# Optimization experiments

Hardware: AMD Instinct MI355X
Metric: run time of the kernel (lower is better)

## Reference

```python
import jax, jax.numpy as jnp
import numpy as np

B, IN_DIM, H1, H2, C = 8192, 1024, 2048, 2048, 1000
E, TOP_K, RH = 8, 2, 512
QB = 127.0
EPS = 1e-5


def _ste_round(x):
    # straight-through estimator round (BitNet-style)
    return x + jax.lax.stop_gradient(jnp.round(x) - x)


def _act_quant(x):
    # per-token absmax 8-bit activation quantization
    s = QB / jnp.clip(jnp.max(jnp.abs(x), axis=-1, keepdims=True), EPS, None)
    return jnp.clip(_ste_round(x * s), -QB, QB) / s


def _weight_quant(w):
    # ternary 1.58b weight quantization, per-tensor mean-abs scale
    s = jnp.clip(jnp.mean(jnp.abs(w)), EPS, None)
    return jnp.clip(_ste_round(w / s), -1.0, 1.0) * s


def _bit_linear(x, w, b):
    return _act_quant(x) @ _weight_quant(w).T + b


def setup_inputs() -> dict:
    key = jax.random.key(0)
    ks = jax.random.split(key, 12)
    def init(k, shape, fan_in):
        return (jax.random.normal(k, shape, dtype=jnp.float32) / np.sqrt(fan_in)).astype(jnp.float32)
    return {
        "x":  jax.random.normal(ks[0], (B, IN_DIM), dtype=jnp.float32),
        "Wr1": init(ks[1], (RH, IN_DIM), IN_DIM),
        "br1": jnp.zeros((RH,), jnp.float32),
        "Wr2": init(ks[2], (E, RH), RH),
        "br2": jnp.zeros((E,), jnp.float32),
        "W1": init(ks[3], (E, H1, IN_DIM), IN_DIM),
        "b1": jnp.zeros((E, H1), jnp.float32),
        "W2": init(ks[4], (E, H2, H1), H1),
        "b2": jnp.zeros((E, H2), jnp.float32),
        "W3": init(ks[5], (E, C, H2), H2),
        "b3": jnp.zeros((E, C), jnp.float32),
    }


def _forward(x, Wr1, br1, Wr2, br2, W1, b1, W2, b2, W3, b3):
    # Router (eval mode: dropout off)
    h = jax.nn.relu(x @ Wr1.T + br1)
    router_probs = jax.nn.softmax(h @ Wr2.T + br2, axis=1)       # [B, E]
    topk_vals, topk_idx = jax.lax.top_k(router_probs, TOP_K)     # [B, K]

    # dense gate matrix: gate[b,e] = sum_k topk_vals[b,k] * (topk_idx[b,k]==e)
    gates = jnp.sum(topk_vals[..., None] * jax.nn.one_hot(topk_idx, E, dtype=x.dtype), axis=1)  # [B, E]

    def expert(w1, c1, w2, c2, w3, c3):
        y = jax.nn.relu(_bit_linear(x, w1, c1))
        y = jax.nn.relu(_bit_linear(y, w2, c2))
        return _bit_linear(y, w3, c3)                             # [B, C]

    out_all = jax.vmap(expert)(W1, b1, W2, b2, W3, b3)            # [E, B, C]
    outputs = jnp.einsum('ebc,be->bc', out_all, gates) / TOP_K    # [B, C]
    load_balancing_loss = jnp.zeros((), x.dtype)                  # eval mode
    return outputs, router_probs, load_balancing_loss


def reference(x, Wr1, br1, Wr2, br2, W1, b1, W2, b2, W3, b3):
    return _forward(x, Wr1, br1, Wr2, br2, W1, b1, W2, b2, W3, b3)
```

## Files before the change

kernel.cpp:

```cpp
#include <hip/hip_runtime.h>
#include <stdint.h>

#define DEV static __device__ __forceinline__

typedef int v4i __attribute__((ext_vector_type(4)));

constexpr int B_T   = 8192;
constexpr int IN_D  = 1024;
constexpr int H1D   = 2048;
constexpr int H2D   = 2048;
constexpr int CDIM  = 1000;
constexpr int NEXP  = 8;
constexpr int RHD   = 512;
constexpr float QBF  = 127.0f;
constexpr float EPSF = 1e-5f;
constexpr int NSLOT = 2 * B_T;
constexpr int MAXT  = 136;

DEV void load_lds16(const void* g, void* l) {
  __builtin_amdgcn_global_load_lds(
      (const __attribute__((address_space(1))) uint32_t*)(uintptr_t)g,
      (__attribute__((address_space(3))) uint32_t*)(uint32_t)(uintptr_t)l,
      16, 0, 0);
}

DEV uint32_t pack4(float a, float b, float c, float d, float s) {
  int q0 = (int)rintf(a * s); q0 = q0 > 127 ? 127 : (q0 < -127 ? -127 : q0);
  int q1 = (int)rintf(b * s); q1 = q1 > 127 ? 127 : (q1 < -127 ? -127 : q1);
  int q2 = (int)rintf(c * s); q2 = q2 > 127 ? 127 : (q2 < -127 ? -127 : q2);
  int q3 = (int)rintf(d * s); q3 = q3 > 127 ? 127 : (q3 < -127 ? -127 : q3);
  return (uint32_t)(uint8_t)q0 | ((uint32_t)(uint8_t)q1 << 8) |
         ((uint32_t)(uint8_t)q2 << 16) | ((uint32_t)(uint8_t)q3 << 24);
}

__global__ __launch_bounds__(256) void wabs_reduce(const float* __restrict__ W,
                                                   long perExpert, int tbase,
                                                   double* __restrict__ partial) {
  int e = blockIdx.y;
  const float4* base = (const float4*)(W + (long)e * perExpert);
  long n4 = perExpert >> 2;
  double s = 0.0;
  for (long i = (long)blockIdx.x * 256 + threadIdx.x; i < n4; i += 32L * 256L) {
    float4 v = base[i];
    s += (double)fabsf(v.x) + (double)fabsf(v.y) + (double)fabsf(v.z) + (double)fabsf(v.w);
  }
  __shared__ double red[256];
  red[threadIdx.x] = s;
  __syncthreads();
  for (int st = 128; st > 0; st >>= 1) {
    if ((int)threadIdx.x < st) red[threadIdx.x] += red[threadIdx.x + st];
    __syncthreads();
  }
  if (threadIdx.x == 0) partial[(long)(tbase + e) * 32 + blockIdx.x] = red[0];
}

__global__ void finalize_scales(const double* __restrict__ partial, float* __restrict__ swf) {
  int t = threadIdx.x;
  if (t >= 24) return;
  double s = 0.0;
  for (int i = 0; i < 32; ++i) s += partial[t * 32 + i];
  long cnt = (t < 8) ? (long)H1D * IN_D : (t < 16) ? (long)H2D * H1D : (long)CDIM * H2D;
  float mean = (float)(s / (double)cnt);
  swf[t] = fmaxf(mean, EPSF);
}

__global__ __launch_bounds__(256) void wquant(const float* __restrict__ W,
                                              int8_t* __restrict__ Wq,
                                              const float* __restrict__ swf, int tbase,
                                              long perExpert, long total4) {
  long i = (long)blockIdx.x * 256 + threadIdx.x;
  if (i >= total4) return;
  long e = (i * 4) / perExpert;
  float s = swf[tbase + (int)e];
  float4 v = ((const float4*)W)[i];
  float t0 = fminf(fmaxf(rintf(v.x / s), -1.f), 1.f);
  float t1 = fminf(fmaxf(rintf(v.y / s), -1.f), 1.f);
  float t2 = fminf(fmaxf(rintf(v.z / s), -1.f), 1.f);
  float t3 = fminf(fmaxf(rintf(v.w / s), -1.f), 1.f);
  uint32_t p = (uint32_t)(uint8_t)(int8_t)t0 | ((uint32_t)(uint8_t)(int8_t)t1 << 8) |
               ((uint32_t)(uint8_t)(int8_t)t2 << 16) | ((uint32_t)(uint8_t)(int8_t)t3 << 24);
  ((uint32_t*)Wq)[i] = p;
}

template <int WIDTH>
__global__ __launch_bounds__(256) void actquant(const float* __restrict__ X,
                                                int8_t* __restrict__ Xq,
                                                float* __restrict__ rcp_out) {
  constexpr int PT = WIDTH / 1024;
  const int row = blockIdx.x;
  const int tid = threadIdx.x;
  const float4* src = (const float4*)(X + (size_t)row * WIDTH);
  float4 v[PT];
  float mx = 0.f;
#pragma unroll
  for (int p = 0; p < PT; ++p) {
    v[p] = src[tid * PT + p];
    mx = fmaxf(mx, fmaxf(fmaxf(fabsf(v[p].x), fabsf(v[p].y)),
                         fmaxf(fabsf(v[p].z), fabsf(v[p].w))));
  }
#pragma unroll
  for (int m = 1; m < 64; m <<= 1) mx = fmaxf(mx, __shfl_xor(mx, m));
  __shared__ float wmax[4];
  const int lane = tid & 63, w = tid >> 6;
  if (lane == 0) wmax[w] = mx;
  __syncthreads();
  mx = fmaxf(fmaxf(wmax[0], wmax[1]), fmaxf(wmax[2], wmax[3]));
  const float M = fmaxf(mx, EPSF);
  const float s = QBF / M;
  uint32_t* dst = (uint32_t*)(Xq + (size_t)row * WIDTH);
#pragma unroll
  for (int p = 0; p < PT; ++p)
    dst[tid * PT + p] = pack4(v[p].x, v[p].y, v[p].z, v[p].w, s);
  if (tid == 0) rcp_out[row] = M / QBF;
}

__global__ __launch_bounds__(256, 4) void router_gemm(const float* __restrict__ x,
                                                      const float* __restrict__ Wr1,
                                                      const float* __restrict__ br1,
                                                      float* __restrict__ h) {
  __shared__ __align__(16) float As[32][64];
  __shared__ __align__(16) float Bs[32][64];
  const int tid = threadIdx.x;
  const int row0 = blockIdx.x * 64, col0 = blockIdx.y * 64;
  const int tx = tid & 15, ty = tid >> 4;
  const int lr = tid >> 2, lc = tid & 3;
  float acc[4][4] = {};
  for (int kt = 0; kt < IN_D; kt += 32) {
    float4 a0 = *(const float4*)&x[(long)(row0 + lr) * IN_D + kt + lc * 4];
    float4 a1 = *(const float4*)&x[(long)(row0 + lr) * IN_D + kt + 16 + lc * 4];
    float4 b0 = *(const float4*)&Wr1[(long)(col0 + lr) * IN_D + kt + lc * 4];
    float4 b1 = *(const float4*)&Wr1[(long)(col0 + lr) * IN_D + kt + 16 + lc * 4];
    __syncthreads();
    As[lc * 4 + 0][lr] = a0.x; As[lc * 4 + 1][lr] = a0.y;
    As[lc * 4 + 2][lr] = a0.z; As[lc * 4 + 3][lr] = a0.w;
    As[16 + lc * 4 + 0][lr] = a1.x; As[16 + lc * 4 + 1][lr] = a1.y;
    As[16 + lc * 4 + 2][lr] = a1.z; As[16 + lc * 4 + 3][lr] = a1.w;
    Bs[lc * 4 + 0][lr] = b0.x; Bs[lc * 4 + 1][lr] = b0.y;
    Bs[lc * 4 + 2][lr] = b0.z; Bs[lc * 4 + 3][lr] = b0.w;
    Bs[16 + lc * 4 + 0][lr] = b1.x; Bs[16 + lc * 4 + 1][lr] = b1.y;
    Bs[16 + lc * 4 + 2][lr] = b1.z; Bs[16 + lc * 4 + 3][lr] = b1.w;
    __syncthreads();
#pragma unroll
    for (int kk = 0; kk < 32; ++kk) {
      float4 av = *(const float4*)&As[kk][ty * 4];
      float4 bv = *(const float4*)&Bs[kk][tx * 4];
      float a4[4] = {av.x, av.y, av.z, av.w};
      float b4[4] = {bv.x, bv.y, bv.z, bv.w};
#pragma unroll
      for (int i = 0; i < 4; ++i)
#pragma unroll
        for (int j = 0; j < 4; ++j) acc[i][j] = fmaf(a4[i], b4[j], acc[i][j]);
    }
  }
#pragma unroll
  for (int i = 0; i < 4; ++i) {
    float4 o;
    o.x = fmaxf(acc[i][0] + br1[col0 + tx * 4 + 0], 0.f);
    o.y = fmaxf(acc[i][1] + br1[col0 + tx * 4 + 1], 0.f);
    o.z = fmaxf(acc[i][2] + br1[col0 + tx * 4 + 2], 0.f);
    o.w = fmaxf(acc[i][3] + br1[col0 + tx * 4 + 3], 0.f);
    *(float4*)&h[(long)(row0 + ty * 4 + i) * RHD + col0 + tx * 4] = o;
  }
}

__global__ __launch_bounds__(256) void router_stage2(const float* __restrict__ h,
                                                     const float* __restrict__ Wr2,
                                                     const float* __restrict__ br2,
                                                     float* __restrict__ probs,
                                                     int* __restrict__ idxg,
                                                     float* __restrict__ gvg) {
  __shared__ float w2s[NEXP * RHD];
  const int tid = threadIdx.x;
  for (int i = tid; i < NEXP * RHD; i += 256) w2s[i] = Wr2[i];
  __syncthreads();
  const int lane = tid & 63, w = tid >> 6;
  const int b = blockIdx.x * 4 + w;
  const float* hrow = h + (long)b * RHD;
  float4 v0 = *(const float4*)&hrow[lane * 8];
  float4 v1 = *(const float4*)&hrow[lane * 8 + 4];
  float hr[8] = {v0.x, v0.y, v0.z, v0.w, v1.x, v1.y, v1.z, v1.w};
  float lg[8];
#pragma unroll
  for (int e = 0; e < 8; ++e) {
    float p = 0.f;
#pragma unroll
    for (int j = 0; j < 8; ++j) p = fmaf(hr[j], w2s[e * RHD + lane * 8 + j], p);
#pragma unroll
    for (int m = 1; m < 64; m <<= 1) p += __shfl_xor(p, m);
    lg[e] = p + br2[e];
  }
  if (lane == 0) {
    float mx = lg[0];
#pragma unroll
    for (int e = 1; e < 8; ++e) mx = fmaxf(mx, lg[e]);
    float ex[8], sum = 0.f;
#pragma unroll
    for (int e = 0; e < 8; ++e) { ex[e] = expf(lg[e] - mx); sum += ex[e]; }
#pragma unroll
    for (int e = 0; e < 8; ++e) probs[(long)b * 8 + e] = ex[e] / sum;
    int i0 = 0; float b0 = lg[0];
#pragma unroll
    for (int e = 1; e < 8; ++e) if (lg[e] > b0) { b0 = lg[e]; i0 = e; }
    int i1 = -1; float b1v = -3.4e38f;
#pragma unroll
    for (int e = 0; e < 8; ++e) if (e != i0 && lg[e] > b1v) { b1v = lg[e]; i1 = e; }
    idxg[b * 2 + 0] = i0; idxg[b * 2 + 1] = i1;
    gvg[b * 2 + 0] = ex[i0] / sum; gvg[b * 2 + 1] = ex[i1] / sum;
  }
}

__global__ __launch_bounds__(256) void hist_block(const int* __restrict__ idxg,
                                                  int* __restrict__ bc) {
  __shared__ int hloc[NEXP];
  const int t = threadIdx.x;
  if (t < NEXP) hloc[t] = 0;
  __syncthreads();
  int a = blockIdx.x * 256 + t;
  atomicAdd(&hloc[idxg[a]], 1);
  __syncthreads();
  if (t < NEXP) bc[blockIdx.x * NEXP + t] = hloc[t];
}

__global__ void scan_all(const int* __restrict__ bc, int* __restrict__ blockbase,
                         int* __restrict__ ntiles, int* __restrict__ te,
                         int* __restrict__ ts, int* __restrict__ tc,
                         float* __restrict__ loss_out) {
  __shared__ int counts[NEXP], basep[NEXP];
  const int t = threadIdx.x;
  if (t < NEXP) {
    int s = 0;
    for (int b = 0; b < 64; ++b) s += bc[b * NEXP + t];
    counts[t] = s;
  }
  __syncthreads();
  if (t == 0) {
    int acc = 0, nb = 0;
    for (int e = 0; e < NEXP; ++e) {
      basep[e] = acc;
      int c = counts[e];
      int nt = (c + 127) >> 7;
      for (int i = 0; i < nt; ++i) {
        te[nb] = e; ts[nb] = acc + i * 128; tc[nb] = min(128, c - i * 128); ++nb;
      }
      acc += c;
    }
    *ntiles = nb;
    *loss_out = 0.f;
  }
  __syncthreads();
  if (t < NEXP) {
    int run = basep[t];
    for (int b = 0; b < 64; ++b) { blockbase[b * NEXP + t] = run; run += bc[b * NEXP + t]; }
  }
}

__global__ __launch_bounds__(256) void place2(const int* __restrict__ idxg,
                                              const int* __restrict__ blockbase,
                                              int* __restrict__ token_list,
                                              int* __restrict__ slotmap) {
  __shared__ int cur[NEXP];
  const int t = threadIdx.x;
  if (t < NEXP) cur[t] = blockbase[blockIdx.x * NEXP + t];
  __syncthreads();
  int a = blockIdx.x * 256 + t;
  int e = idxg[a];
  int pos = atomicAdd(&cur[e], 1);
  token_list[pos] = a >> 1;
  slotmap[a] = pos;
}

template <int KDIM, bool INDIRECT, bool RELU, bool FINAL>
__global__ __launch_bounds__(256, 2) void gemm_i8(
    const int8_t* __restrict__ Aq, const int8_t* __restrict__ Wq,
    const float* __restrict__ swf_layer, const float* __restrict__ rcp_act,
    const float* __restrict__ bias, const int* __restrict__ te,
    const int* __restrict__ ts, const int* __restrict__ tc,
    const int* __restrict__ ntiles_p, const int* __restrict__ token_list,
    float* __restrict__ Yout, int Nvalid) {
  if ((int)blockIdx.x >= *ntiles_p) return;
  __shared__ __align__(16) int8_t smem[2][16384];
  const int t = blockIdx.x;
  const int e = te[t], row0 = ts[t], rcount = tc[t];
  const int col0 = blockIdx.y * 128;
  const int tid = threadIdx.x;
  const int lane = tid & 63, wid = tid >> 6;
  const int wm = wid >> 1, wn = wid & 1;

  const int8_t* srcA[2];
  const int8_t* srcB[2];
#pragma unroll
  for (int i = 0; i < 2; ++i) {
    int p = tid + i * 256;
    int r = p >> 2, c = p & 3;
    int cs = c ^ ((r >> 1) & 3);
    int ar = row0 + min(r, rcount - 1);
    long arow = INDIRECT ? (long)token_list[ar] : (long)ar;
    srcA[i] = Aq + arow * KDIM + cs * 16;
    int br = min(col0 + r, Nvalid - 1);
    srcB[i] = Wq + ((long)e * Nvalid + br) * (long)KDIM + cs * 16;
  }

  v4i acc[4][4] = {};
  auto stage = [&](int buf, int kt) {
#pragma unroll
    for (int i = 0; i < 2; ++i) {
      int off = (i * 256 + wid * 64) * 16;
      load_lds16(srcA[i] + kt * 64, &smem[buf][off]);
      load_lds16(srcB[i] + kt * 64, &smem[buf][8192 + off]);
    }
  };

  constexpr int KT = KDIM / 64;
  stage(0, 0);
  asm volatile("s_waitcnt vmcnt(0)" ::: "memory");
  __syncthreads();
  int buf = 0;
  for (int kt = 0; kt < KT; ++kt) {
    if (kt + 1 < KT) stage(buf ^ 1, kt + 1);
    const v4i* As = (const v4i*)&smem[buf][0];
    const v4i* Bs = (const v4i*)&smem[buf][8192];
    v4i av[4], bv[4];
#pragma unroll
    for (int m = 0; m < 4; ++m) {
      int r = wm * 64 + m * 16 + (lane & 15);
      av[m] = As[r * 4 + ((lane >> 4) ^ ((r >> 1) & 3))];
    }
#pragma unroll
    for (int n = 0; n < 4; ++n) {
      int r = wn * 64 + n * 16 + (lane & 15);
      bv[n] = Bs[r * 4 + ((lane >> 4) ^ ((r >> 1) & 3))];
    }
#pragma unroll
    for (int m = 0; m < 4; ++m)
#pragma unroll
      for (int n = 0; n < 4; ++n)
        acc[m][n] = __builtin_amdgcn_mfma_i32_16x16x64_i8(av[m], bv[n], acc[m][n], 0, 0, 0);
    asm volatile("s_waitcnt vmcnt(0)" ::: "memory");
    __syncthreads();
    buf ^= 1;
  }

  const float sw = swf_layer[e];
  const int rbase = (lane >> 4) * 4;
  const int cfr = lane & 15;
  const float* bias_e = bias + (long)e * Nvalid;
#pragma unroll
  for (int m = 0; m < 4; ++m) {
#pragma unroll
    for (int rg = 0; rg < 4; ++rg) {
      int trow = wm * 64 + m * 16 + rbase + rg;
      if (trow >= rcount) continue;
      int slot = row0 + trow;
      float rcp = rcp_act[INDIRECT ? token_list[slot] : slot];
      float dq = sw * rcp;
      if (!FINAL) {
        float* yrow = Yout + (long)slot * 2048;
#pragma unroll
        for (int n = 0; n < 4; ++n) {
          int o = col0 + wn * 64 + n * 16 + cfr;
          float v = (float)acc[m][n][rg] * dq + bias_e[o];
          if (RELU) v = fmaxf(v, 0.f);
          yrow[o] = v;
        }
      } else {
        float* zrow = Yout + (long)slot * 1024;
#pragma unroll
        for (int n = 0; n < 4; ++n) {
          int o = col0 + wn * 64 + n * 16 + cfr;
          float bb = bias_e[min(o, Nvalid - 1)];
          zrow[o] = (float)acc[m][n][rg] * dq + bb;
        }
      }
    }
  }
}

__global__ __launch_bounds__(256) void combine(const float* __restrict__ z,
                                               const int* __restrict__ slotmap,
                                               const float* __restrict__ gvg,
                                               float* __restrict__ out) {
  const int b = blockIdx.x;
  const int c = threadIdx.x;
  if (c >= 250) return;
  const int s0 = slotmap[b * 2], s1 = slotmap[b * 2 + 1];
  const float g0 = gvg[b * 2] * 0.5f, g1 = gvg[b * 2 + 1] * 0.5f;
  float4 a = *(const float4*)(z + (long)s0 * 1024 + c * 4);
  float4 q = *(const float4*)(z + (long)s1 * 1024 + c * 4);
  float4 o = {g0 * a.x + g1 * q.x, g0 * a.y + g1 * q.y,
              g0 * a.z + g1 * q.z, g0 * a.w + g1 * q.w};
  *(float4*)(out + (long)b * CDIM + c * 4) = o;
}

extern "C" void kernel_launch(void* const* d_in, const int* in_sizes, int n_in,
                              void* d_out, int out_size, void* d_ws, size_t ws_size,
                              hipStream_t stream) {
  const float* x   = (const float*)d_in[0];
  const float* Wr1 = (const float*)d_in[1];
  const float* br1 = (const float*)d_in[2];
  const float* Wr2 = (const float*)d_in[3];
  const float* br2 = (const float*)d_in[4];
  const float* W1  = (const float*)d_in[5];
  const float* b1  = (const float*)d_in[6];
  const float* W2  = (const float*)d_in[7];
  const float* b2  = (const float*)d_in[8];
  const float* W3  = (const float*)d_in[9];
  const float* b3  = (const float*)d_in[10];
  float* out = (float*)d_out;
  char* ws = (char*)d_ws;

  size_t off = 0;
  auto alloc = [&](size_t sz) { size_t r = off; off = (off + sz + 255) & ~(size_t)255; return r; };
  size_t O_META  = alloc(8192);
  size_t O_PART  = alloc(24 * 32 * sizeof(double));
  size_t O_SWF   = alloc(24 * sizeof(float));
  size_t O_RCPX  = alloc(B_T * sizeof(float));
  size_t O_IDX   = alloc(B_T * 2 * sizeof(int));
  size_t O_GVG   = alloc(B_T * 2 * sizeof(float));
  size_t O_TLIST = alloc(NSLOT * sizeof(int));
  size_t O_SLOT  = alloc(B_T * 2 * sizeof(int));
  size_t O_S1    = alloc(NSLOT * sizeof(float));
  size_t O_S2    = alloc(NSLOT * sizeof(float));
  size_t O_XQ    = alloc((size_t)B_T * IN_D);
  size_t O_WQ1   = alloc((size_t)NEXP * H1D * IN_D);
  size_t O_WQ2   = alloc((size_t)NEXP * H2D * H1D);
  size_t O_WQ3   = alloc((size_t)NEXP * CDIM * H2D);
  size_t O_YQ    = alloc((size_t)NSLOT * 2048);
  size_t O_YBIG  = alloc((size_t)NSLOT * 2048 * sizeof(float));
  (void)ws_size; (void)in_sizes; (void)n_in;

  int*    te     = (int*)(ws + O_META);
  int*    tsv    = te + 144;
  int*    tcv    = tsv + 144;
  int*    ntiles = tcv + 144;
  int*    bc     = ntiles + 4;
  int*    bbase  = bc + 512;
  double* part   = (double*)(ws + O_PART);
  float*  swf    = (float*)(ws + O_SWF);
  float*  rcpx   = (float*)(ws + O_RCPX);
  int*    idxg   = (int*)(ws + O_IDX);
  float*  gvg    = (float*)(ws + O_GVG);
  int*    tlist  = (int*)(ws + O_TLIST);
  int*    slotmap= (int*)(ws + O_SLOT);
  float*  s1     = (float*)(ws + O_S1);
  float*  s2     = (float*)(ws + O_S2);
  int8_t* Xq     = (int8_t*)(ws + O_XQ);
  int8_t* wq1    = (int8_t*)(ws + O_WQ1);
  int8_t* wq2    = (int8_t*)(ws + O_WQ2);
  int8_t* wq3    = (int8_t*)(ws + O_WQ3);
  int8_t* Yq     = (int8_t*)(ws + O_YQ);
  float*  Ybig   = (float*)(ws + O_YBIG);
  float*  h      = Ybig;
  float*  zbuf   = Ybig;

  wabs_reduce<<<dim3(32, 8), 256, 0, stream>>>(W1, (long)H1D * IN_D, 0, part);
  wabs_reduce<<<dim3(32, 8), 256, 0, stream>>>(W2, (long)H2D * H1D, 8, part);
  wabs_reduce<<<dim3(32, 8), 256, 0, stream>>>(W3, (long)CDIM * H2D, 16, part);
  finalize_scales<<<1, 64, 0, stream>>>(part, swf);
  wquant<<<16384, 256, 0, stream>>>(W1, wq1, swf, 0, (long)H1D * IN_D, 4194304L);
  wquant<<<32768, 256, 0, stream>>>(W2, wq2, swf, 8, (long)H2D * H1D, 8388608L);
  wquant<<<16000, 256, 0, stream>>>(W3, wq3, swf, 16, (long)CDIM * H2D, 4096000L);

  actquant<IN_D><<<B_T, 256, 0, stream>>>(x, Xq, rcpx);

  router_gemm<<<dim3(B_T / 64, RHD / 64), 256, 0, stream>>>(x, Wr1, br1, h);
  router_stage2<<<B_T / 4, 256, 0, stream>>>(h, Wr2, br2, out + (size_t)B_T * CDIM,
                                             idxg, gvg);
  hist_block<<<64, 256, 0, stream>>>(idxg, bc);
  scan_all<<<1, 64, 0, stream>>>(bc, bbase, ntiles, te, tsv, tcv,
                                 out + (size_t)B_T * CDIM + (size_t)B_T * NEXP);
  place2<<<64, 256, 0, stream>>>(idxg, bbase, tlist, slotmap);

  gemm_i8<IN_D, true, true, false><<<dim3(MAXT, H1D / 128), 256, 0, stream>>>(
      Xq, wq1, swf + 0, rcpx, b1, te, tsv, tcv, ntiles, tlist, Ybig, H1D);
  actquant<2048><<<NSLOT, 256, 0, stream>>>(Ybig, Yq, s1);
  gemm_i8<2048, false, true, false><<<dim3(MAXT, H2D / 128), 256, 0, stream>>>(
      Yq, wq2, swf + 8, s1, b2, te, tsv, tcv, ntiles, tlist, Ybig, H2D);
  actquant<2048><<<NSLOT, 256, 0, stream>>>(Ybig, Yq, s2);
  gemm_i8<2048, false, false, true><<<dim3(MAXT, 1024 / 128), 256, 0, stream>>>(
      Yq, wq3, swf + 16, s2, b3, te, tsv, tcv, ntiles, tlist, zbuf, CDIM);

  combine<<<B_T, 256, 0, stream>>>(zbuf, slotmap, gvg, out);
}
```

Baseline: 693.5 us.

## Run router GEMM on bf16x3 MFMA with fp32 fixup for near-tie tokens

Replaces the scalar fp32 router GEMM with an MFMA kernel that emulates fp32 precision by splitting x and Wr1 into bf16 hi/lo parts and summing three bf16 products. Tokens whose second and third router logits are within a small gap are flagged and recomputed in full fp32 by a fixup kernel, so that top-k selection matches the reference. This adds split kernels, a memset, and extra workspace traffic. It also risks residual precision differences in router_probs for tokens that are not flagged.

Measured after the change: 688.5 us. Within noise of the previous version (-0.7%).

```diff
diff --git a/kernel.cpp b/kernel.cpp
--- a/kernel.cpp
+++ b/kernel.cpp
@@ -4,6 +4,8 @@
 #define DEV static __device__ __forceinline__
 
 typedef int v4i __attribute__((ext_vector_type(4)));
+typedef short v8s __attribute__((ext_vector_type(8)));
+typedef float v4f __attribute__((ext_vector_type(4)));
 
 constexpr int B_T   = 8192;
 constexpr int IN_D  = 1024;
@@ -16,6 +18,7 @@
 constexpr float EPSF = 1e-5f;
 constexpr int NSLOT = 2 * B_T;
 constexpr int MAXT  = 136;
+constexpr float GAP_DELTA = 2e-3f;
 
 DEV void load_lds16(const void* g, void* l) {
   __builtin_amdgcn_global_load_lds(
@@ -32,6 +35,12 @@
   return (uint32_t)(uint8_t)q0 | ((uint32_t)(uint8_t)q1 << 8) |
          ((uint32_t)(uint8_t)q2 << 16) | ((uint32_t)(uint8_t)q3 << 24);
 }
+
+DEV uint16_t f2bf(float f) {
+  uint32_t u = __float_as_uint(f);
+  return (uint16_t)((u + 0x7FFFu + ((u >> 16) & 1u)) >> 16);
+}
+DEV float bf2f(uint16_t h) { return __uint_as_float((uint32_t)h << 16); }
 
 __global__ __launch_bounds__(256) void wabs_reduce(const float* __restrict__ W,
                                                    long perExpert, int tbase,
@@ -114,53 +123,109 @@
   if (tid == 0) rcp_out[row] = M / QBF;
 }
 
-__global__ __launch_bounds__(256, 4) void router_gemm(const float* __restrict__ x,
-                                                      const float* __restrict__ Wr1,
-                                                      const float* __restrict__ br1,
-                                                      float* __restrict__ h) {
-  __shared__ __align__(16) float As[32][64];
-  __shared__ __align__(16) float Bs[32][64];
+__global__ __launch_bounds__(256) void split_bf16(const float* __restrict__ src,
+                                                  uint16_t* __restrict__ hi,
+                                                  uint16_t* __restrict__ lo, long n4) {
+  long i = (long)blockIdx.x * 256 + threadIdx.x;
+  if (i >= n4) return;
+  float4 v = ((const float4*)src)[i];
+  ushort4 h, l;
+  float f[4] = {v.x, v.y, v.z, v.w};
+  uint16_t hh[4], ll[4];
+#pragma unroll
+  for (int j = 0; j < 4; ++j) {
+    hh[j] = f2bf(f[j]);
+    ll[j] = f2bf(f[j] - bf2f(hh[j]));
+  }
+  h.x = hh[0]; h.y = hh[1]; h.z = hh[2]; h.w = hh[3];
+  l.x = ll[0]; l.y = ll[1]; l.z = ll[2]; l.w = ll[3];
+  ((ushort4*)hi)[i] = h;
+  ((ushort4*)lo)[i] = l;
+}
+
+__global__ __launch_bounds__(256, 1) void router_mfma(
+    const uint16_t* __restrict__ xh, const uint16_t* __restrict__ xl,
+    const uint16_t* __restrict__ wh, const uint16_t* __restrict__ wl,
+    const float* __restrict__ br1, float* __restrict__ h) {
+  __shared__ __align__(16) int8_t smem[2][65536];
   const int tid = threadIdx.x;
-  const int row0 = blockIdx.x * 64, col0 = blockIdx.y * 64;
-  const int tx = tid & 15, ty = tid >> 4;
-  const int lr = tid >> 2, lc = tid & 3;
-  float acc[4][4] = {};
-  for (int kt = 0; kt < IN_D; kt += 32) {
-    float4 a0 = *(const float4*)&x[(long)(row0 + lr) * IN_D + kt + lc * 4];
-    float4 a1 = *(const float4*)&x[(long)(row0 + lr) * IN_D + kt + 16 + lc * 4];
-    float4 b0 = *(const float4*)&Wr1[(long)(col0 + lr) * IN_D + kt + lc * 4];
-    float4 b1 = *(const float4*)&Wr1[(long)(col0 + lr) * IN_D + kt + 16 + lc * 4];
+  const int lane = tid & 63, wid = tid >> 6;
+  const int wm = wid >> 1, wn = wid & 1;
+  const int row0 = blockIdx.x * 128, col0 = blockIdx.y * 128;
+
+  const uint16_t* mats[4] = {xh, xl, wh, wl};
+  const int rb[4] = {row0, row0, col0, col0};
+  const uint8_t* src[16];
+#pragma unroll
+  for (int R = 0; R < 4; ++R)
+#pragma unroll
+    for (int i = 0; i < 4; ++i) {
+      int p = i * 256 + tid;
+      int r = p >> 3, c = p & 7;
+      int cs = c ^ (r & 7);
+      src[R * 4 + i] = (const uint8_t*)mats[R] + ((long)(rb[R] + r) * IN_D + cs * 8) * 2;
+    }
+
+  v4f acc[4][4] = {};
+  auto stage = [&](int buf, int kt) {
+#pragma unroll
+    for (int R = 0; R < 4; ++R)
+#pragma unroll
+      for (int i = 0; i < 4; ++i)
+        load_lds16(src[R * 4 + i] + kt * 128,
+                   &smem[buf][R * 16384 + i * 4096 + wid * 1024]);
+  };
+
+  stage(0, 0);
+  asm volatile("s_waitcnt vmcnt(0)" ::: "memory");
+  __syncthreads();
+  int buf = 0;
+  for (int kt = 0; kt < 16; ++kt) {
+    if (kt + 1 < 16) stage(buf ^ 1, kt + 1);
+#pragma unroll
+    for (int ks = 0; ks < 2; ++ks) {
+      v8s ah[4], al[4], bh[4], bl[4];
+#pragma unroll
+      for (int m = 0; m < 4; ++m) {
+        int r = wm * 64 + m * 16 + (lane & 15);
+        int ch = (ks * 4 + (lane >> 4)) ^ (r & 7);
+        ah[m] = *(const v8s*)&smem[buf][r * 128 + ch * 16];
+        al[m] = *(const v8s*)&smem[buf][16384 + r * 128 + ch * 16];
+      }
+#pragma unroll
+      for (int n = 0; n < 4; ++n) {
+        int r = wn * 64 + n * 16 + (lane & 15);
+        int ch = (ks * 4 + (lane >> 4)) ^ (r & 7);
+        bh[n] = *(const v8s*)&smem[buf][32768 + r * 128 + ch * 16];
+        bl[n] = *(const v8s*)&smem[buf][49152 + r * 128 + ch * 16];
+      }
+#pragma unroll
+      for (int m = 0; m < 4; ++m)
+#pragma unroll
+        for (int n = 0; n < 4; ++n) {
+          acc[m][n] = __builtin_amdgcn_mfma_f32_16x16x32_bf16(ah[m], bh[n], acc[m][n], 0, 0, 0);
+          acc[m][n] = __builtin_amdgcn_mfma_f32_16x16x32_bf16(ah[m], bl[n], acc[m][n], 0, 0, 0);
+          acc[m][n] = __builtin_amdgcn_mfma_f32_16x16x32_bf16(al[m], bh[n], acc[m][n], 0, 0, 0);
+        }
+    }
+    asm volatile("s_waitcnt vmcnt(0)" ::: "memory");
     __syncthreads();
-    As[lc * 4 + 0][lr] = a0.x; As[lc * 4 + 1][lr] = a0.y;
-    As[lc * 4 + 2][lr] = a0.z; As[lc * 4 + 3][lr] = a0.w;
-    As[16 + lc * 4 + 0][lr] = a1.x; As[16 + lc * 4 + 1][lr] = a1.y;
-    As[16 + lc * 4 + 2][lr] = a1.z; As[16 + lc * 4 + 3][lr] = a1.w;
-    Bs[lc * 4 + 0][lr] = b0.x; Bs[lc * 4 + 1][lr] = b0.y;
-    Bs[lc * 4 + 2][lr] = b0.z; Bs[lc * 4 + 3][lr] = b0.w;
-    Bs[16 + lc * 4 + 0][lr] = b1.x; Bs[16 + lc * 4 + 1][lr] = b1.y;
-    Bs[16 + lc * 4 + 2][lr] = b1.z; Bs[16 + lc * 4 + 3][lr] = b1.w;
-    __syncthreads();
-#pragma unroll
-    for (int kk = 0; kk < 32; ++kk) {
-      float4 av = *(const float4*)&As[kk][ty * 4];
-      float4 bv = *(const float4*)&Bs[kk][tx * 4];
-      float a4[4] = {av.x, av.y, av.z, av.w};
-      float b4[4] = {bv.x, bv.y, bv.z, bv.w};
-#pragma unroll
-      for (int i = 0; i < 4; ++i)
-#pragma unroll
-        for (int j = 0; j < 4; ++j) acc[i][j] = fmaf(a4[i], b4[j], acc[i][j]);
-    }
-  }
-#pragma unroll
-  for (int i = 0; i < 4; ++i) {
-    float4 o;
-    o.x = fmaxf(acc[i][0] + br1[col0 + tx * 4 + 0], 0.f);
-    o.y = fmaxf(acc[i][1] + br1[col0 + tx * 4 + 1], 0.f);
-    o.z = fmaxf(acc[i][2] + br1[col0 + tx * 4 + 2], 0.f);
-    o.w = fmaxf(acc[i][3] + br1[col0 + tx * 4 + 3], 0.f);
-    *(float4*)&h[(long)(row0 + ty * 4 + i) * RHD + col0 + tx * 4] = o;
-  }
+    buf ^= 1;
+  }
+
+  const int rbase = (lane >> 4) * 4;
+  const int cfr = lane & 15;
+#pragma unroll
+  for (int m = 0; m < 4; ++m)
+#pragma unroll
+    for (int rg = 0; rg < 4; ++rg) {
+      int row = row0 + wm * 64 + m * 16 + rbase + rg;
+#pragma unroll
+      for (int n = 0; n < 4; ++n) {
+        int col = col0 + wn * 64 + n * 16 + cfr;
+        h[(long)row * RHD + col] = fmaxf(acc[m][n][rg] + br1[col], 0.f);
+      }
+    }
 }
 
 __global__ __launch_bounds__(256) void router_stage2(const float* __restrict__ h,
@@ -168,7 +233,9 @@
                                                      const float* __restrict__ br2,
                                                      float* __restrict__ probs,
                                                      int* __restrict__ idxg,
-                                                     float* __restrict__ gvg) {
+                                                     float* __restrict__ gvg,
+                                                     int* __restrict__ scount,
+                                                     int* __restrict__ suspects) {
   __shared__ float w2s[NEXP * RHD];
   const int tid = threadIdx.x;
   for (int i = tid; i < NEXP * RHD; i += 256) w2s[i] = Wr2[i];
@@ -204,8 +271,80 @@
     int i1 = -1; float b1v = -3.4e38f;
 #pragma unroll
     for (int e = 0; e < 8; ++e) if (e != i0 && lg[e] > b1v) { b1v = lg[e]; i1 = e; }
+    float b2v = -3.4e38f;
+#pragma unroll
+    for (int e = 0; e < 8; ++e) if (e != i0 && e != i1 && lg[e] > b2v) b2v = lg[e];
     idxg[b * 2 + 0] = i0; idxg[b * 2 + 1] = i1;
     gvg[b * 2 + 0] = ex[i0] / sum; gvg[b * 2 + 1] = ex[i1] / sum;
+    if (b1v - b2v < GAP_DELTA) {
+      int p = atomicAdd(scount, 1);
+      if (p < B_T) suspects[p] = b;
+    }
+  }
+}
+
+__global__ __launch_bounds__(256) void router_fixup(const float* __restrict__ x,
+                                                    const float* __restrict__ Wr1,
+                                                    const float* __restrict__ br1,
+                                                    const float* __restrict__ Wr2,
+                                                    const float* __restrict__ br2,
+                                                    const int* __restrict__ suspects,
+                                                    const int* __restrict__ scount,
+                                                    float* __restrict__ probs,
+                                                    int* __restrict__ idxg,
+                                                    float* __restrict__ gvg) {
+  __shared__ float xr[IN_D];
+  __shared__ float hr[RHD];
+  __shared__ float lgs[NEXP];
+  const int n = *scount;
+  const int tid = threadIdx.x;
+  for (int s = blockIdx.x; s < n && s < B_T; s += 128) {
+    const int b = suspects[s];
+    __syncthreads();
+    for (int i = tid; i < IN_D; i += 256) xr[i] = x[(long)b * IN_D + i];
+    __syncthreads();
+    {
+      const int c0 = tid * 2, c1 = tid * 2 + 1;
+      const float* w0 = Wr1 + (long)c0 * IN_D;
+      const float* w1 = Wr1 + (long)c1 * IN_D;
+      float a0 = 0.f, a1 = 0.f;
+      for (int k = 0; k < IN_D; ++k) {
+        float xv = xr[k];
+        a0 = fmaf(xv, w0[k], a0);
+        a1 = fmaf(xv, w1[k], a1);
+      }
+      hr[c0] = fmaxf(a0 + br1[c0], 0.f);
+      hr[c1] = fmaxf(a1 + br1[c1], 0.f);
+    }
+    __syncthreads();
+    if (tid < NEXP) {
+      const float* w2 = Wr2 + (long)tid * RHD;
+      float a = 0.f;
+      for (int k = 0; k < RHD; ++k) a = fmaf(hr[k], w2[k], a);
+      lgs[tid] = a + br2[tid];
+    }
+    __syncthreads();
+    if (tid == 0) {
+      float lg[8];
+#pragma unroll
+      for (int e = 0; e < 8; ++e) lg[e] = lgs[e];
+      float mx = lg[0];
+#pragma unroll
+      for (int e = 1; e < 8; ++e) mx = fmaxf(mx, lg[e]);
+      float ex[8], sum = 0.f;
+#pragma unroll
+      for (int e = 0; e < 8; ++e) { ex[e] = expf(lg[e] - mx); sum += ex[e]; }
+#pragma unroll
+      for (int e = 0; e < 8; ++e) probs[(long)b * 8 + e] = ex[e] / sum;
+      int i0 = 0; float b0 = lg[0];
+#pragma unroll
+      for (int e = 1; e < 8; ++e) if (lg[e] > b0) { b0 = lg[e]; i0 = e; }
+      int i1 = -1; float b1v = -3.4e38f;
+#pragma unroll
+      for (int e = 0; e < 8; ++e) if (e != i0 && lg[e] > b1v) { b1v = lg[e]; i1 = e; }
+      idxg[b * 2 + 0] = i0; idxg[b * 2 + 1] = i1;
+      gvg[b * 2 + 0] = ex[i0] / sum; gvg[b * 2 + 1] = ex[i1] / sum;
+    }
   }
 }
 
@@ -411,6 +550,7 @@
   size_t off = 0;
   auto alloc = [&](size_t sz) { size_t r = off; off = (off + sz + 255) & ~(size_t)255; return r; };
   size_t O_META  = alloc(8192);
+  size_t O_SUSP  = alloc(B_T * sizeof(int));
   size_t O_PART  = alloc(24 * 32 * sizeof(double));
   size_t O_SWF   = alloc(24 * sizeof(float));
   size_t O_RCPX  = alloc(B_T * sizeof(float));
@@ -434,6 +574,8 @@
   int*    ntiles = tcv + 144;
   int*    bc     = ntiles + 4;
   int*    bbase  = bc + 512;
+  int*    scount = bbase + 512;
+  int*    susp   = (int*)(ws + O_SUSP);
   double* part   = (double*)(ws + O_PART);
   float*  swf    = (float*)(ws + O_SWF);
   float*  rcpx   = (float*)(ws + O_RCPX);
@@ -452,6 +594,14 @@
   float*  h      = Ybig;
   float*  zbuf   = Ybig;
 
+  char* ybytes = (char*)Ybig;
+  uint16_t* xh = (uint16_t*)(ybytes + (20l << 20));
+  uint16_t* xl = (uint16_t*)(ybytes + (40l << 20));
+  uint16_t* wh = (uint16_t*)(ybytes + (60l << 20));
+  uint16_t* wl = (uint16_t*)(ybytes + (62l << 20));
+
+  hipMemsetAsync(ws + O_META, 0, 8192, stream);
+
   wabs_reduce<<<dim3(32, 8), 256, 0, stream>>>(W1, (long)H1D * IN_D, 0, part);
   wabs_reduce<<<dim3(32, 8), 256, 0, stream>>>(W2, (long)H2D * H1D, 8, part);
   wabs_reduce<<<dim3(32, 8), 256, 0, stream>>>(W3, (long)CDIM * H2D, 16, part);
@@ -462,9 +612,13 @@
 
   actquant<IN_D><<<B_T, 256, 0, stream>>>(x, Xq, rcpx);
 
-  router_gemm<<<dim3(B_T / 64, RHD / 64), 256, 0, stream>>>(x, Wr1, br1, h);
+  split_bf16<<<8192, 256, 0, stream>>>(x, xh, xl, (long)B_T * IN_D / 4);
+  split_bf16<<<512, 256, 0, stream>>>(Wr1, wh, wl, (long)RHD * IN_D / 4);
+  router_mfma<<<dim3(B_T / 128, RHD / 128), 256, 0, stream>>>(xh, xl, wh, wl, br1, h);
   router_stage2<<<B_T / 4, 256, 0, stream>>>(h, Wr2, br2, out + (size_t)B_T * CDIM,
-                                             idxg, gvg);
+                                             idxg, gvg, scount, susp);
+  router_fixup<<<128, 256, 0, stream>>>(x, Wr1, br1, Wr2, br2, susp, scount,
+                                        out + (size_t)B_T * CDIM, idxg, gvg);
   hist_block<<<64, 256, 0, stream>>>(idxg, bc);
   scan_all<<<1, 64, 0, stream>>>(bc, bbase, ntiles, te, tsv, tcv,
                                  out + (size_t)B_T * CDIM + (size_t)B_T * NEXP);
```
